# Optimization experiments

Hardware: AMD Instinct MI355X
Metric: run time of the kernel (lower is better)

## Reference

```python
import jax, jax.numpy as jnp
import numpy as np

TOP_K = 4
ALPHA = 1.702
LIMIT = 7.0


def setup_inputs() -> dict:
    key = jax.random.key(0)
    ks = jax.random.split(key, 7)
    B, S, H, I, E = 1, 512, 2880, 2880, 16
    s = 0.02
    return {
        "hidden_states": jax.random.normal(ks[0], (B, S, H), dtype=jnp.float32),
        "router_w": jax.random.normal(ks[1], (H, E), dtype=jnp.float32) * s,
        "router_b": jax.random.normal(ks[2], (E,), dtype=jnp.float32) * s,
        "gate_up_w": jax.random.normal(ks[3], (E, H, 2 * I), dtype=jnp.float32) * s,
        "gate_up_b": jax.random.normal(ks[4], (E, 2 * I), dtype=jnp.float32) * s,
        "down_w": jax.random.normal(ks[5], (E, I, H), dtype=jnp.float32) * s,
        "down_b": jax.random.normal(ks[6], (E, H), dtype=jnp.float32) * s,
    }


def reference(hidden_states, router_w, router_b, gate_up_w, gate_up_b, down_w, down_b):
    B, S, H = hidden_states.shape
    x = hidden_states.reshape(-1, H)                      # [T, H]
    T = x.shape[0]

    # Router: top-k + softmax over selected logits, scattered back to [T, E]
    router_logits = x @ router_w + router_b               # [T, E]
    top_v, top_i = jax.lax.top_k(router_logits, TOP_K)    # [T, K]
    top_v = jax.nn.softmax(top_v, axis=-1)
    router_scores = jnp.zeros_like(router_logits).at[
        jnp.arange(T)[:, None], top_i
    ].set(top_v)                                          # [T, E]

    # Dense all-experts GLU (matches the repeat-across-experts formulation)
    gate_up = jnp.einsum('th,ehd->etd', x, gate_up_w) + gate_up_b[:, None, :]  # [E, T, 2I]
    gate = gate_up[..., ::2]                              # [E, T, I]
    up = gate_up[..., 1::2]                               # [E, T, I]
    gate = jnp.minimum(gate, LIMIT)
    up = jnp.clip(up, -LIMIT, LIMIT)
    glu = gate * jax.nn.sigmoid(gate * ALPHA)
    expert_out = jnp.einsum('eti,eih->eth', (up + 1.0) * glu, down_w) + down_b[:, None, :]  # [E, T, H]

    # Masked combine with routing weights
    out = jnp.sum(expert_out * router_scores.T[:, :, None], axis=0)  # [T, H]
    return (out.reshape(B, S, H),)
```

## Files before the change

kernel.cpp:

```cpp
#include <hip/hip_runtime.h>
#include <hip/hip_bf16.h>

#define NTOK 512
#define HDIM 2880
#define NGU  5760
#define NEXP 16
#define KSTEPS 90
#define KSH   45
#define MT 160
#define MFR 10
#define PARTELT ((size_t)(NTOK*4) * HDIM)

typedef float  f32x4  __attribute__((ext_vector_type(4)));
typedef float  f32x2  __attribute__((ext_vector_type(2)));
typedef short  bf16x8 __attribute__((ext_vector_type(8)));

__device__ __forceinline__ unsigned short f2bf(float f) {
  union { float f; unsigned u; } a; a.f = f;
  unsigned r = a.u + 0x7FFFu + ((a.u >> 16) & 1u);
  return (unsigned short)(r >> 16);
}

__device__ __forceinline__ void lds_barrier() {
  asm volatile("s_waitcnt lgkmcnt(0)" ::: "memory");
  __builtin_amdgcn_s_barrier();
  asm volatile("" ::: "memory");
}


__global__ __launch_bounds__(256) void k_router(
    const float* __restrict__ x, const float* __restrict__ rw,
    const float* __restrict__ rb, int* __restrict__ counts,
    int* __restrict__ top_e, float* __restrict__ top_w)
{
  const int t = blockIdx.x;
  const int tid = threadIdx.x;
  __shared__ float red[256][17];
  float acc[NEXP];
#pragma unroll
  for (int e = 0; e < NEXP; ++e) acc[e] = 0.f;
  const float* xr = x + (size_t)t * HDIM;
  for (int h = tid; h < HDIM; h += 256) {
    float xv = xr[h];
    const f32x4* wr = (const f32x4*)(rw + (size_t)h * NEXP);
#pragma unroll
    for (int q = 0; q < 4; ++q) {
      f32x4 w = wr[q];
#pragma unroll
      for (int j = 0; j < 4; ++j) acc[q*4+j] += xv * w[j];
    }
  }
#pragma unroll
  for (int e = 0; e < NEXP; ++e) red[tid][e] = acc[e];
  __syncthreads();
  for (int s = 128; s > 0; s >>= 1) {
    if (tid < s) {
#pragma unroll
      for (int e = 0; e < NEXP; ++e) red[tid][e] += red[tid + s][e];
    }
    __syncthreads();
  }
  if (tid == 0) {
    float v[NEXP];
#pragma unroll
    for (int e = 0; e < NEXP; ++e) v[e] = red[0][e] + rb[e];
    int mask = 0; float tv[4]; int ti[4];
    for (int k = 0; k < 4; ++k) {
      float best = -3.4e38f; int bi = 0;
      for (int e = 0; e < NEXP; ++e)
        if (!((mask >> e) & 1) && v[e] > best) { best = v[e]; bi = e; }
      mask |= 1 << bi; tv[k] = best; ti[k] = bi;
    }
    float s = 0.f, ex[4];
    for (int k = 0; k < 4; ++k) { ex[k] = __expf(tv[k] - tv[0]); s += ex[k]; }
    float inv = 1.f / s;
    for (int k = 0; k < 4; ++k) {
      top_e[t*4+k] = ti[k];
      top_w[t*4+k] = ex[k] * inv;
      atomicAdd(&counts[ti[k]], 1);
    }
  }
}

__global__ __launch_bounds__(64) void k_fill(
    const int* __restrict__ top_e, const float* __restrict__ top_w,
    const int* __restrict__ counts, int* __restrict__ seg,
    int* __restrict__ pair_tok, float* __restrict__ pair_w,
    int* __restrict__ pair_of)
{
  const int e = blockIdx.x;
  const int lane = threadIdx.x;
  int base = 0;
  for (int i = 0; i < e; ++i) base += counts[i];
  if (lane == 0) {
    seg[e] = base;
    if (e == NEXP - 1) seg[NEXP] = base + counts[e];
  }
  for (int t0 = 0; t0 < NTOK; t0 += 64) {
    int t = t0 + lane;
    int my = -1;
#pragma unroll
    for (int k = 0; k < 4; ++k) if (top_e[t*4+k] == e) my = k;
    unsigned long long m = __ballot(my >= 0);
    if (my >= 0) {
      int pre = __popcll(m & ((1ull << lane) - 1ull));
      pair_tok[base + pre] = t;
      pair_w[base + pre] = top_w[t*4+my];
      pair_of[t*4 + my] = base + pre;
    }
    base += (int)__popcll(m);
  }
}

__global__ __launch_bounds__(256) void k_xbf16(
    const float* __restrict__ x, unsigned short* __restrict__ xb,
    int* __restrict__ counts)
{
  if (blockIdx.x == 0 && threadIdx.x < NEXP) counts[threadIdx.x] = 0;
  int i = (blockIdx.x * 256 + threadIdx.x) * 8;
  f32x4 a = *(const f32x4*)(x + i);
  f32x4 b = *(const f32x4*)(x + i + 4);
  bf16x8 o;
#pragma unroll
  for (int j = 0; j < 4; ++j) { o[j] = (short)f2bf(a[j]); o[4+j] = (short)f2bf(b[j]); }
  *(bf16x8*)(xb + i) = o;
}

__global__ __launch_bounds__(256, 2) void k_gateup(
    const unsigned short* __restrict__ xb, const float* __restrict__ gw,
    const float* __restrict__ gb, const int* __restrict__ seg,
    const int* __restrict__ pair_tok, const float* __restrict__ pair_w,
    unsigned short* __restrict__ act)
{
  const int e = blockIdx.z;
  const int segs = seg[e];
  const int n_e = seg[e+1] - segs;
  const int m0 = blockIdx.y * MT;
  if (m0 >= n_e) return;
  const int tid = threadIdx.x;
  const int lane = tid & 63;
  const int wid = tid >> 6;
  const int l15 = lane & 15, lg = lane >> 4;
  const int fcb = blockIdx.x * 128 + wid * 32;
  const int fcE = fcb + 2*l15;
  const int colf = min(2*fcb + 4*l15, NGU - 4);

  __shared__ unsigned short Alds[2][MT][40];

  const float* Bq = gw + (size_t)e * HDIM * NGU + colf + (size_t)lg * 8 * NGU;

  const unsigned short* sp0 = nullptr;
  const unsigned short* sp1 = nullptr;
  const int r0 = tid >> 1, h0 = tid & 1;
  const int r1 = (tid + 256) >> 1, h1 = tid & 1;
  if (m0 + r0 < n_e) sp0 = xb + (size_t)pair_tok[segs + m0 + r0] * HDIM + h0*16;
  if (tid < 2*MT - 256 && m0 + r1 < n_e)
    sp1 = xb + (size_t)pair_tok[segs + m0 + r1] * HDIM + h1*16;

  f32x4 accgE[MFR], accuE[MFR], accgO[MFR], accuO[MFR];
  {
    f32x4 b = __builtin_nontemporal_load((const f32x4*)(gb + (size_t)e * NGU + colf));
#pragma unroll
    for (int m = 0; m < MFR; ++m)
#pragma unroll
      for (int r = 0; r < 4; ++r) {
        accgE[m][r] = b[0]; accuE[m][r] = b[1];
        accgO[m][r] = b[2]; accuO[m][r] = b[3];
      }
  }

  auto stage = [&](int ks, int b) {
    bf16x8 z = {0,0,0,0,0,0,0,0};
    bf16x8 v0 = z, v1 = z;
    if (sp0) { v0 = *(const bf16x8*)(sp0 + ks*32); v1 = *(const bf16x8*)(sp0 + ks*32 + 8); }
    *(bf16x8*)&Alds[b][r0][h0*16]     = v0;
    *(bf16x8*)&Alds[b][r0][h0*16 + 8] = v1;
    if (tid < 2*MT - 256) {
      bf16x8 w0 = z, w1 = z;
      if (sp1) { w0 = *(const bf16x8*)(sp1 + ks*32); w1 = *(const bf16x8*)(sp1 + ks*32 + 8); }
      *(bf16x8*)&Alds[b][r1][h1*16]     = w0;
      *(bf16x8*)&Alds[b][r1][h1*16 + 8] = w1;
    }
  };

  f32x4 bA[8];
  auto loadB = [&](int ks) {
    const float* bp = Bq + (size_t)ks * 32 * NGU;
#pragma unroll
    for (int j = 0; j < 8; ++j)
      bA[j] = __builtin_nontemporal_load((const f32x4*)(bp + (size_t)j * NGU));
  };

  loadB(0);
  stage(0, 0);
  lds_barrier();
  int buf = 0;

  for (int ks = 0; ks < KSTEPS; ++ks) {
    if (ks + 1 < KSTEPS) stage(ks + 1, buf ^ 1);
    bf16x8 bgE, buE, bgO, buO;
#pragma unroll
    for (int j = 0; j < 8; ++j) {
      bgE[j] = (short)f2bf(bA[j][0]); buE[j] = (short)f2bf(bA[j][1]);
      bgO[j] = (short)f2bf(bA[j][2]); buO[j] = (short)f2bf(bA[j][3]);
    }
    if (ks + 1 < KSTEPS) loadB(ks + 1);
#pragma unroll
    for (int m = 0; m < MFR; ++m) {
      bf16x8 a = *(const bf16x8*)&Alds[buf][m*16 + l15][lg*8];
      accgE[m] = __builtin_amdgcn_mfma_f32_16x16x32_bf16(a, bgE, accgE[m], 0, 0, 0);
      accuE[m] = __builtin_amdgcn_mfma_f32_16x16x32_bf16(a, buE, accuE[m], 0, 0, 0);
      accgO[m] = __builtin_amdgcn_mfma_f32_16x16x32_bf16(a, bgO, accgO[m], 0, 0, 0);
      accuO[m] = __builtin_amdgcn_mfma_f32_16x16x32_bf16(a, buO, accuO[m], 0, 0, 0);
    }
    lds_barrier();
    buf ^= 1;
  }

  if (fcE < HDIM) {
#pragma unroll
    for (int m = 0; m < MFR; ++m) {
#pragma unroll
      for (int r = 0; r < 4; ++r) {
        int grow = m0 + m*16 + lg*4 + r;
        if (grow < n_e) {
          float pw = pair_w[segs + grow];
          float gE = fminf(accgE[m][r], 7.f);
          float uE = fminf(fmaxf(accuE[m][r], -7.f), 7.f);
          float avE = (uE + 1.f) * (gE / (1.f + __expf(-1.702f * gE))) * pw;
          float gO = fminf(accgO[m][r], 7.f);
          float uO = fminf(fmaxf(accuO[m][r], -7.f), 7.f);
          float avO = (uO + 1.f) * (gO / (1.f + __expf(-1.702f * gO))) * pw;
          unsigned pk = (unsigned)f2bf(avE) | ((unsigned)f2bf(avO) << 16);
          *(unsigned*)&act[(size_t)(segs + grow) * HDIM + fcE] = pk;
        }
      }
    }
  }
}

__global__ __launch_bounds__(256, 3) void k_down(
    const unsigned short* __restrict__ act, const float* __restrict__ dw,
    const int* __restrict__ seg, const int* __restrict__ pair_tok,
    float* __restrict__ partial)
{
  const int e = blockIdx.z;
  const int mi = blockIdx.y >> 1;
  const int kh = blockIdx.y & 1;
  const int segs = seg[e];
  const int n_e = seg[e+1] - segs;
  const int m0 = mi * MT;
  if (m0 >= n_e) return;
  const int tid = threadIdx.x;
  const int lane = tid & 63;
  const int wid = tid >> 6;
  const int l15 = lane & 15, lg = lane >> 4;
  const int cb = blockIdx.x * 128 + wid * 32;
  const int cE = cb + 2*l15;
  const int colc = min(cE, HDIM - 2);
  const int k0 = kh * (KSH * 32);

  __shared__ unsigned short Alds[2][MT][40];

  float* po = partial + (size_t)kh * PARTELT;
  const float* Bq = dw + (size_t)e * HDIM * HDIM + colc
                  + (size_t)(k0 + lg * 8) * HDIM;

  const unsigned short* sp0 = nullptr;
  const unsigned short* sp1 = nullptr;
  const int r0 = tid >> 1, h0 = tid & 1;
  const int r1 = (tid + 256) >> 1, h1 = tid & 1;
  if (m0 + r0 < n_e) sp0 = act + (size_t)(segs + m0 + r0) * HDIM + k0 + h0*16;
  if (tid < 2*MT - 256 && m0 + r1 < n_e)
    sp1 = act + (size_t)(segs + m0 + r1) * HDIM + k0 + h1*16;

  f32x4 accE[MFR], accO[MFR];
#pragma unroll
  for (int m = 0; m < MFR; ++m)
#pragma unroll
    for (int r = 0; r < 4; ++r) { accE[m][r] = 0.f; accO[m][r] = 0.f; }

  auto stage = [&](int ks, int b) {
    bf16x8 z = {0,0,0,0,0,0,0,0};
    bf16x8 v0 = z, v1 = z;
    if (sp0) { v0 = *(const bf16x8*)(sp0 + ks*32); v1 = *(const bf16x8*)(sp0 + ks*32 + 8); }
    *(bf16x8*)&Alds[b][r0][h0*16]     = v0;
    *(bf16x8*)&Alds[b][r0][h0*16 + 8] = v1;
    if (tid < 2*MT - 256) {
      bf16x8 w0 = z, w1 = z;
      if (sp1) { w0 = *(const bf16x8*)(sp1 + ks*32); w1 = *(const bf16x8*)(sp1 + ks*32 + 8); }
      *(bf16x8*)&Alds[b][r1][h1*16]     = w0;
      *(bf16x8*)&Alds[b][r1][h1*16 + 8] = w1;
    }
  };

  f32x2 bA[8];
  auto loadB = [&](int ks) {
    const float* bp = Bq + (size_t)ks * 32 * HDIM;
#pragma unroll
    for (int j = 0; j < 8; ++j)
      bA[j] = __builtin_nontemporal_load((const f32x2*)(bp + (size_t)j * HDIM));
  };

  loadB(0);
  stage(0, 0);
  lds_barrier();
  int buf = 0;

  for (int ks = 0; ks < KSH; ++ks) {
    if (ks + 1 < KSH) stage(ks + 1, buf ^ 1);
    bf16x8 bfE, bfO;
#pragma unroll
    for (int j = 0; j < 8; ++j) { bfE[j] = (short)f2bf(bA[j][0]); bfO[j] = (short)f2bf(bA[j][1]); }
    if (ks + 1 < KSH) loadB(ks + 1);
#pragma unroll
    for (int m = 0; m < MFR; ++m) {
      bf16x8 a = *(const bf16x8*)&Alds[buf][m*16 + l15][lg*8];
      accE[m] = __builtin_amdgcn_mfma_f32_16x16x32_bf16(a, bfE, accE[m], 0, 0, 0);
      accO[m] = __builtin_amdgcn_mfma_f32_16x16x32_bf16(a, bfO, accO[m], 0, 0, 0);
    }
    lds_barrier();
    buf ^= 1;
  }

  if (cE < HDIM) {
#pragma unroll
    for (int m = 0; m < MFR; ++m) {
#pragma unroll
      for (int r = 0; r < 4; ++r) {
        int grow = m0 + m*16 + lg*4 + r;
        if (grow < n_e) {
          f32x2 v = { accE[m][r], accO[m][r] };
          *(f32x2*)&po[(size_t)(segs + grow) * HDIM + cE] = v;
        }
      }
    }
  }
}

__global__ __launch_bounds__(256) void k_gather(
    const float* __restrict__ partial, const int* __restrict__ pair_of,
    const int* __restrict__ top_e, const float* __restrict__ top_w,
    const float* __restrict__ db, float* __restrict__ out)
{
  const int t = blockIdx.x;
  const int tid = threadIdx.x;
  const int p0 = pair_of[t*4+0], p1 = pair_of[t*4+1];
  const int p2 = pair_of[t*4+2], p3 = pair_of[t*4+3];
  const float w0 = top_w[t*4+0], w1 = top_w[t*4+1];
  const float w2 = top_w[t*4+2], w3 = top_w[t*4+3];
  const float* r0 = partial + (size_t)p0 * HDIM;
  const float* r1 = partial + (size_t)p1 * HDIM;
  const float* r2 = partial + (size_t)p2 * HDIM;
  const float* r3 = partial + (size_t)p3 * HDIM;
  const float* q0 = r0 + PARTELT;
  const float* q1 = r1 + PARTELT;
  const float* q2 = r2 + PARTELT;
  const float* q3 = r3 + PARTELT;
  const float* b0 = db + (size_t)top_e[t*4+0] * HDIM;
  const float* b1 = db + (size_t)top_e[t*4+1] * HDIM;
  const float* b2 = db + (size_t)top_e[t*4+2] * HDIM;
  const float* b3 = db + (size_t)top_e[t*4+3] * HDIM;
  float* o = out + (size_t)t * HDIM;
  for (int p = tid; p < HDIM/4; p += 256) {
    f32x4 v0 = *(const f32x4*)(r0 + 4*p);
    f32x4 v1 = *(const f32x4*)(r1 + 4*p);
    f32x4 v2 = *(const f32x4*)(r2 + 4*p);
    f32x4 v3 = *(const f32x4*)(r3 + 4*p);
    f32x4 u0 = *(const f32x4*)(q0 + 4*p);
    f32x4 u1 = *(const f32x4*)(q1 + 4*p);
    f32x4 u2 = *(const f32x4*)(q2 + 4*p);
    f32x4 u3 = *(const f32x4*)(q3 + 4*p);
    f32x4 c0 = *(const f32x4*)(b0 + 4*p);
    f32x4 c1 = *(const f32x4*)(b1 + 4*p);
    f32x4 c2 = *(const f32x4*)(b2 + 4*p);
    f32x4 c3 = *(const f32x4*)(b3 + 4*p);
    f32x4 s;
#pragma unroll
    for (int j = 0; j < 4; ++j)
      s[j] = ((v0[j] + u0[j]) + (v1[j] + u1[j]))
           + ((v2[j] + u2[j]) + (v3[j] + u3[j]))
           + (w0*c0[j] + w1*c1[j]) + (w2*c2[j] + w3*c3[j]);
    *(f32x4*)(o + 4*p) = s;
  }
}


extern "C" void kernel_launch(void* const* d_in, const int* in_sizes, int n_in,
                              void* d_out, int out_size, void* d_ws, size_t ws_size,
                              hipStream_t stream) {
  const float* x  = (const float*)d_in[0];
  const float* rw = (const float*)d_in[1];
  const float* rb = (const float*)d_in[2];
  const float* gw = (const float*)d_in[3];
  const float* gb = (const float*)d_in[4];
  const float* dw = (const float*)d_in[5];
  const float* db = (const float*)d_in[6];
  float* out = (float*)d_out;

  char* w = (char*)d_ws;
  int*   counts   = (int*)(w);
  int*   seg      = (int*)(w + 64);
  int*   top_e    = (int*)(w + 1024);
  float* top_w    = (float*)(w + 1024 + 8192);
  int*   pair_tok = (int*)(w + 1024 + 16384);
  float* pair_w   = (float*)(w + 1024 + 24576);
  int*   pair_of  = (int*)(w + 1024 + 32768);
  unsigned short* xb  = (unsigned short*)(w + (1 << 20));
  unsigned short* act = (unsigned short*)(w + (8 << 20));
  float* partial = (float*)(w + (64ull << 20));

  k_xbf16<<<(NTOK*HDIM)/(256*8), 256, 0, stream>>>(x, xb, counts);
  k_router<<<NTOK, 256, 0, stream>>>(x, rw, rb, counts, top_e, top_w);
  k_fill<<<NEXP, 64, 0, stream>>>(top_e, top_w, counts, seg, pair_tok, pair_w, pair_of);

  dim3 gg(23, 2, NEXP);
  k_gateup<<<gg, 256, 0, stream>>>(xb, gw, gb, seg, pair_tok, pair_w, act);

  dim3 gd(23, 4, NEXP);
  k_down<<<gd, 256, 0, stream>>>(act, dw, seg, pair_tok, partial);

  k_gather<<<NTOK, 256, 0, stream>>>(partial, pair_of, top_e, top_w, db, out);
}
```

Baseline: 437.5 us.

## Split gate-up GEMM along K into two halves with separate activation kernel

The gate-up kernel now splits the hidden (K) dimension into two halves across blockIdx.z, doubling the number of blocks. Each half writes fp32 partial gate/up sums to a workspace buffer. A new k_act kernel adds the halves, applies clamp, SwiGLU and the routing weight, and packs the result to bf16. This is meant to give the weight-streaming GEMM more parallelism to fill the GPU. In exchange it adds an extra launch and roughly 90 MB of fp32 partial-sum writes and reads.

```diff
diff --git a/kernel.cpp b/kernel.cpp
--- a/kernel.cpp
+++ b/kernel.cpp
@@ -9,6 +9,7 @@
 #define KSH   45
 #define MT 160
 #define MFR 10
+#define GUELT   ((size_t)(NTOK*4) * NGU)
 #define PARTELT ((size_t)(NTOK*4) * HDIM)
 
 typedef float  f32x4  __attribute__((ext_vector_type(4)));
@@ -129,10 +130,10 @@
 __global__ __launch_bounds__(256, 2) void k_gateup(
     const unsigned short* __restrict__ xb, const float* __restrict__ gw,
     const float* __restrict__ gb, const int* __restrict__ seg,
-    const int* __restrict__ pair_tok, const float* __restrict__ pair_w,
-    unsigned short* __restrict__ act)
-{
-  const int e = blockIdx.z;
+    const int* __restrict__ pair_tok, float* __restrict__ gu)
+{
+  const int e  = blockIdx.z >> 1;
+  const int kh = blockIdx.z & 1;
   const int segs = seg[e];
   const int n_e = seg[e+1] - segs;
   const int m0 = blockIdx.y * MT;
@@ -144,22 +145,27 @@
   const int fcb = blockIdx.x * 128 + wid * 32;
   const int fcE = fcb + 2*l15;
   const int colf = min(2*fcb + 4*l15, NGU - 4);
+  const int k0 = kh * (KSH * 32);
 
   __shared__ unsigned short Alds[2][MT][40];
 
-  const float* Bq = gw + (size_t)e * HDIM * NGU + colf + (size_t)lg * 8 * NGU;
+  float* gup = gu + (size_t)kh * GUELT;
+  const float* Bq = gw + (size_t)e * HDIM * NGU + colf
+                  + (size_t)(k0 + lg * 8) * NGU;
 
   const unsigned short* sp0 = nullptr;
   const unsigned short* sp1 = nullptr;
   const int r0 = tid >> 1, h0 = tid & 1;
   const int r1 = (tid + 256) >> 1, h1 = tid & 1;
-  if (m0 + r0 < n_e) sp0 = xb + (size_t)pair_tok[segs + m0 + r0] * HDIM + h0*16;
+  if (m0 + r0 < n_e) sp0 = xb + (size_t)pair_tok[segs + m0 + r0] * HDIM + k0 + h0*16;
   if (tid < 2*MT - 256 && m0 + r1 < n_e)
-    sp1 = xb + (size_t)pair_tok[segs + m0 + r1] * HDIM + h1*16;
+    sp1 = xb + (size_t)pair_tok[segs + m0 + r1] * HDIM + k0 + h1*16;
 
   f32x4 accgE[MFR], accuE[MFR], accgO[MFR], accuO[MFR];
   {
-    f32x4 b = __builtin_nontemporal_load((const f32x4*)(gb + (size_t)e * NGU + colf));
+    f32x4 b = {0.f, 0.f, 0.f, 0.f};
+    if (kh == 0)
+      b = __builtin_nontemporal_load((const f32x4*)(gb + (size_t)e * NGU + colf));
 #pragma unroll
     for (int m = 0; m < MFR; ++m)
 #pragma unroll
@@ -196,15 +202,15 @@
   lds_barrier();
   int buf = 0;
 
-  for (int ks = 0; ks < KSTEPS; ++ks) {
-    if (ks + 1 < KSTEPS) stage(ks + 1, buf ^ 1);
+  for (int ks = 0; ks < KSH; ++ks) {
+    if (ks + 1 < KSH) stage(ks + 1, buf ^ 1);
     bf16x8 bgE, buE, bgO, buO;
 #pragma unroll
     for (int j = 0; j < 8; ++j) {
       bgE[j] = (short)f2bf(bA[j][0]); buE[j] = (short)f2bf(bA[j][1]);
       bgO[j] = (short)f2bf(bA[j][2]); buO[j] = (short)f2bf(bA[j][3]);
     }
-    if (ks + 1 < KSTEPS) loadB(ks + 1);
+    if (ks + 1 < KSH) loadB(ks + 1);
 #pragma unroll
     for (int m = 0; m < MFR; ++m) {
       bf16x8 a = *(const bf16x8*)&Alds[buf][m*16 + l15][lg*8];
@@ -224,18 +230,34 @@
       for (int r = 0; r < 4; ++r) {
         int grow = m0 + m*16 + lg*4 + r;
         if (grow < n_e) {
-          float pw = pair_w[segs + grow];
-          float gE = fminf(accgE[m][r], 7.f);
-          float uE = fminf(fmaxf(accuE[m][r], -7.f), 7.f);
-          float avE = (uE + 1.f) * (gE / (1.f + __expf(-1.702f * gE))) * pw;
-          float gO = fminf(accgO[m][r], 7.f);
-          float uO = fminf(fmaxf(accuO[m][r], -7.f), 7.f);
-          float avO = (uO + 1.f) * (gO / (1.f + __expf(-1.702f * gO))) * pw;
-          unsigned pk = (unsigned)f2bf(avE) | ((unsigned)f2bf(avO) << 16);
-          *(unsigned*)&act[(size_t)(segs + grow) * HDIM + fcE] = pk;
+          f32x4 v = { accgE[m][r], accuE[m][r], accgO[m][r], accuO[m][r] };
+          *(f32x4*)&gup[(size_t)(segs + grow) * NGU + colf] = v;
         }
       }
     }
+  }
+}
+
+__global__ __launch_bounds__(256) void k_act(
+    const float* __restrict__ gu, const float* __restrict__ pair_w,
+    unsigned short* __restrict__ act)
+{
+  const int row = blockIdx.x;
+  const float w = pair_w[row];
+  const float* a = gu + (size_t)row * NGU;
+  const float* b = gu + GUELT + (size_t)row * NGU;
+  unsigned short* o = act + (size_t)row * HDIM;
+  for (int p = threadIdx.x; p < HDIM/2; p += 256) {
+    f32x4 va = *(const f32x4*)(a + 4*p);
+    f32x4 vb = *(const f32x4*)(b + 4*p);
+    float g0 = va[0] + vb[0], u0 = va[1] + vb[1];
+    float g1 = va[2] + vb[2], u1 = va[3] + vb[3];
+    g0 = fminf(g0, 7.f); u0 = fminf(fmaxf(u0, -7.f), 7.f);
+    g1 = fminf(g1, 7.f); u1 = fminf(fmaxf(u1, -7.f), 7.f);
+    float av0 = (u0 + 1.f) * (g0 / (1.f + __expf(-1.702f * g0))) * w;
+    float av1 = (u1 + 1.f) * (g1 / (1.f + __expf(-1.702f * g1))) * w;
+    unsigned pk = (unsigned)f2bf(av0) | ((unsigned)f2bf(av1) << 16);
+    *(unsigned*)&o[2*p] = pk;
   }
 }
 
@@ -408,14 +430,17 @@
   int*   pair_of  = (int*)(w + 1024 + 32768);
   unsigned short* xb  = (unsigned short*)(w + (1 << 20));
   unsigned short* act = (unsigned short*)(w + (8 << 20));
-  float* partial = (float*)(w + (64ull << 20));
+  float* partial = (float*)(w + (24ull << 20));
+  float* gu      = (float*)(w + (80ull << 20));
 
   k_xbf16<<<(NTOK*HDIM)/(256*8), 256, 0, stream>>>(x, xb, counts);
   k_router<<<NTOK, 256, 0, stream>>>(x, rw, rb, counts, top_e, top_w);
   k_fill<<<NEXP, 64, 0, stream>>>(top_e, top_w, counts, seg, pair_tok, pair_w, pair_of);
 
-  dim3 gg(23, 2, NEXP);
-  k_gateup<<<gg, 256, 0, stream>>>(xb, gw, gb, seg, pair_tok, pair_w, act);
+  dim3 gg(23, 2, NEXP * 2);
+  k_gateup<<<gg, 256, 0, stream>>>(xb, gw, gb, seg, pair_tok, gu);
+
+  k_act<<<NTOK*4, 256, 0, stream>>>(gu, pair_w, act);
 
   dim3 gd(23, 4, NEXP);
   k_down<<<gd, 256, 0, stream>>>(act, dw, seg, pair_tok, partial);
```

New measurement: 469.9 us. 1.07x slower.
